# Kernel tuning notes

Hardware: AMD Instinct MI355X
Metric: run time of the kernel (lower is better)

The kernel has to match this reference:

```python
import jax, jax.numpy as jnp
import numpy as np

N = 100000   # nodes
E = 1600000  # edges (before self-loops)
H1, C1 = 8, 16   # conv1: heads=8, out_channels=16
H2, C2 = 1, 1    # conv2: heads=1, out_channels=1
NEG_SLOPE = 0.2
EPS = 1e-16


def setup_inputs() -> dict:
    key = jax.random.key(0)
    ks = jax.random.split(key, 10)
    s = 0.3
    return {
        "x": jax.random.normal(ks[0], (N, 1), jnp.float32),
        "edge_index": jax.random.randint(ks[1], (2, E), 0, N, dtype=jnp.int64),
        "W1": jax.random.normal(ks[2], (1, H1 * C1), jnp.float32) * s,
        "att_src1": jax.random.normal(ks[3], (1, H1, C1), jnp.float32) * s,
        "att_dst1": jax.random.normal(ks[4], (1, H1, C1), jnp.float32) * s,
        "b1": jax.random.normal(ks[5], (H1 * C1,), jnp.float32) * s,
        "W2": jax.random.normal(ks[6], (H1 * C1, H2 * C2), jnp.float32) * s,
        "att_src2": jax.random.normal(ks[7], (1, H2, C2), jnp.float32) * s,
        "att_dst2": jax.random.normal(ks[8], (1, H2, C2), jnp.float32) * s,
        "b2": jax.random.normal(ks[9], (C2,), jnp.float32) * s,
    }


def gat_conv(x, src, dst, W, att_src, att_dst, bias, heads, ch, concat):
    # Linear projection, split into heads: [N, H, C]
    h = (x @ W).reshape(-1, heads, ch)
    # Per-node attention logits: [N, H]
    a_src = (h * att_src).sum(-1)
    a_dst = (h * att_dst).sum(-1)
    # Edge-wise score with LeakyReLU: [E, H]
    e = jax.nn.leaky_relu(a_src[src] + a_dst[dst], NEG_SLOPE)
    # Segment softmax over incoming edges of each dst node
    m = jax.ops.segment_max(e, dst, num_segments=N)
    ex = jnp.exp(e - m[dst])
    denom = jax.ops.segment_sum(ex, dst, num_segments=N)
    alpha = ex / (denom[dst] + EPS)                      # [E, H]
    # Weighted scatter-add aggregation: [N, H, C]
    out = jax.ops.segment_sum(h[src] * alpha[:, :, None], dst, num_segments=N)
    out = out.reshape(-1, heads * ch) if concat else out.mean(axis=1)
    return out + bias


def reference(x, edge_index, W1, att_src1, att_dst1, b1, W2, att_src2, att_dst2, b2):
    # PyG GATConv default add_self_loops=True
    loop = jnp.arange(N, dtype=edge_index.dtype)
    src = jnp.concatenate([edge_index[0], loop])
    dst = jnp.concatenate([edge_index[1], loop])
    # dropout p=0.6 is identity in eval mode
    h = gat_conv(x, src, dst, W1, att_src1, att_dst1, b1, H1, C1, concat=True)
    h = jax.nn.elu(h)
    out = gat_conv(h, src, dst, W2, att_src2, att_dst2, b2, H2, C2, concat=False)
    return out  # [N, 1]
```

## Files before the change

### kernel.cpp

```cpp
#include <hip/hip_runtime.h>

#define NEG_SLOPE 0.2f
#define EPSV 1e-16f
#define NHEADS 8
#define NCH 16
#define BKT_SHIFT 8
#define BKT_NODES 256
#define CAP 8192
#define BIN_EPB 4096
#define MAX_BKT 512

__global__ __launch_bounds__(512) void gat_setup_kernel(
        const float* __restrict__ W1, const float* __restrict__ as1,
        const float* __restrict__ ad1, float* __restrict__ S1,
        float* __restrict__ D1, int* __restrict__ bkt_cnt, int nbuckets) {
    int t = threadIdx.x;
    for (int i = t; i < nbuckets; i += 512) bkt_cnt[i] = 0;
    if (t < NHEADS) {
        float s = 0.f, d = 0.f;
        for (int c = 0; c < NCH; ++c) {
            float w = W1[t * NCH + c];
            s += w * as1[t * NCH + c];
            d += w * ad1[t * NCH + c];
        }
        S1[t] = s;
        D1[t] = d;
    }
}

__global__ __launch_bounds__(256) void gat_bin_kernel(
        const int* __restrict__ ei, int E, int nbuckets,
        int* __restrict__ bkt_cnt, unsigned int* __restrict__ binned) {
    __shared__ int hist[MAX_BKT];
    __shared__ int gbase[MAX_BKT];
    int t = threadIdx.x;
    for (int i = t; i < nbuckets; i += 256) hist[i] = 0;
    __syncthreads();
    int base = blockIdx.x * BIN_EPB;
    int lr[BIN_EPB / 256];
#pragma unroll
    for (int k = 0; k < BIN_EPB / 1024; ++k) {
        int idx = base + k * 1024 + t * 4;
        if (idx + 3 < E) {
            int4 d4 = *(const int4*)(ei + E + idx);
            lr[4 * k + 0] = atomicAdd(&hist[d4.x >> BKT_SHIFT], 1);
            lr[4 * k + 1] = atomicAdd(&hist[d4.y >> BKT_SHIFT], 1);
            lr[4 * k + 2] = atomicAdd(&hist[d4.z >> BKT_SHIFT], 1);
            lr[4 * k + 3] = atomicAdd(&hist[d4.w >> BKT_SHIFT], 1);
        } else {
            for (int u = 0; u < 4; ++u)
                if (idx + u < E)
                    lr[4 * k + u] = atomicAdd(&hist[ei[E + idx + u] >> BKT_SHIFT], 1);
        }
    }
    __syncthreads();
    for (int i = t; i < nbuckets; i += 256) {
        int c = hist[i];
        gbase[i] = c ? (i * CAP + atomicAdd(&bkt_cnt[i], c)) : 0;
    }
    __syncthreads();
#pragma unroll
    for (int k = 0; k < BIN_EPB / 1024; ++k) {
        int idx = base + k * 1024 + t * 4;
        if (idx + 3 < E) {
            int4 s4 = *(const int4*)(ei + idx);
            int4 d4 = *(const int4*)(ei + E + idx);
            binned[gbase[d4.x >> BKT_SHIFT] + lr[4 * k + 0]] =
                ((unsigned int)s4.x << BKT_SHIFT) | (unsigned int)(d4.x & (BKT_NODES - 1));
            binned[gbase[d4.y >> BKT_SHIFT] + lr[4 * k + 1]] =
                ((unsigned int)s4.y << BKT_SHIFT) | (unsigned int)(d4.y & (BKT_NODES - 1));
            binned[gbase[d4.z >> BKT_SHIFT] + lr[4 * k + 2]] =
                ((unsigned int)s4.z << BKT_SHIFT) | (unsigned int)(d4.z & (BKT_NODES - 1));
            binned[gbase[d4.w >> BKT_SHIFT] + lr[4 * k + 3]] =
                ((unsigned int)s4.w << BKT_SHIFT) | (unsigned int)(d4.w & (BKT_NODES - 1));
        } else {
            for (int u = 0; u < 4; ++u)
                if (idx + u < E) {
                    unsigned int s = (unsigned int)ei[idx + u];
                    int d = ei[E + idx + u];
                    binned[gbase[d >> BKT_SHIFT] + lr[4 * k + u]] =
                        (s << BKT_SHIFT) | (unsigned int)(d & (BKT_NODES - 1));
                }
        }
    }
}

__global__ __launch_bounds__(256) void gat_gather1_kernel(
        int N, const float* __restrict__ x,
        unsigned int* __restrict__ binned, const int* __restrict__ bkt_cnt,
        const float* __restrict__ S1g, const float* __restrict__ D1g,
        const float* __restrict__ W1, const float* __restrict__ b1,
        const float* __restrict__ W2, float* __restrict__ h2out,
        int* __restrict__ row_start, int* __restrict__ row_deg) {
    __shared__ unsigned int ed[CAP];
    __shared__ int cnt[BKT_NODES];
    __shared__ int off[BKT_NODES];
    __shared__ int cur[BKT_NODES];
    __shared__ float xloc[BKT_NODES];
    int b = blockIdx.x, t = threadIdx.x;
    int node = (b << BKT_SHIFT) + t;
    xloc[t] = (node < N) ? x[node] : 0.f;
    cnt[t] = 0;
    __syncthreads();
    int nE = bkt_cnt[b]; if (nE > CAP) nE = CAP;
    const unsigned int* bb = binned + (size_t)b * CAP;
    for (int j0 = 0; j0 < nE; j0 += 1024) {
        int idx = j0 + t * 4;
        if (idx + 3 < nE) {
            uint4 q = *(const uint4*)(bb + idx);
            atomicAdd(&cnt[q.x & (BKT_NODES - 1)], 1);
            atomicAdd(&cnt[q.y & (BKT_NODES - 1)], 1);
            atomicAdd(&cnt[q.z & (BKT_NODES - 1)], 1);
            atomicAdd(&cnt[q.w & (BKT_NODES - 1)], 1);
        } else {
            for (int u = 0; u < 4; ++u)
                if (idx + u < nE) atomicAdd(&cnt[bb[idx + u] & (BKT_NODES - 1)], 1);
        }
    }
    __syncthreads();
    int c = cnt[t];
    off[t] = c;
    __syncthreads();
    for (int o = 1; o < 256; o <<= 1) {
        int v = (t >= o) ? off[t - o] : 0;
        __syncthreads();
        off[t] += v;
        __syncthreads();
    }
    int o_excl = off[t] - c;
    off[t] = o_excl;
    cur[t] = o_excl;
    __syncthreads();
    for (int j0 = 0; j0 < nE; j0 += 1024) {
        int idx = j0 + t * 4;
        if (idx + 3 < nE) {
            uint4 q = *(const uint4*)(bb + idx);
            ed[atomicAdd(&cur[q.x & (BKT_NODES - 1)], 1)] = q.x >> BKT_SHIFT;
            ed[atomicAdd(&cur[q.y & (BKT_NODES - 1)], 1)] = q.y >> BKT_SHIFT;
            ed[atomicAdd(&cur[q.z & (BKT_NODES - 1)], 1)] = q.z >> BKT_SHIFT;
            ed[atomicAdd(&cur[q.w & (BKT_NODES - 1)], 1)] = q.w >> BKT_SHIFT;
        } else {
            for (int u = 0; u < 4; ++u)
                if (idx + u < nE) {
                    unsigned int v = bb[idx + u];
                    ed[atomicAdd(&cur[v & (BKT_NODES - 1)], 1)] = v >> BKT_SHIFT;
                }
        }
    }
    __syncthreads();
    for (int j0 = 0; j0 < nE; j0 += 1024) {
        int idx = j0 + t * 4;
        if (idx + 3 < nE) {
            *(uint4*)(binned + (size_t)b * CAP + idx) = *(const uint4*)(ed + idx);
        } else {
            for (int u = 0; u < 4; ++u)
                if (idx + u < nE) binned[(size_t)b * CAP + idx + u] = ed[idx + u];
        }
    }
    if (node < N) {
        row_start[node] = b * CAP + o_excl;
        row_deg[node] = c;
    }
    float S1[NHEADS], A[NHEADS], den[NHEADS], num[NHEADS];
    float xn = xloc[t];
#pragma unroll
    for (int h = 0; h < NHEADS; ++h) {
        S1[h] = S1g[h];
        A[h] = xn * D1g[h];
        float e = xn * S1[h] + A[h];
        e = e > 0.f ? e : NEG_SLOPE * e;
        float ex = __expf(e);
        den[h] = ex + EPSV;
        num[h] = ex * xn;
    }
    int j = 0;
    for (; j + 4 <= c; j += 4) {
        unsigned int e0 = ed[o_excl + j + 0], e1 = ed[o_excl + j + 1];
        unsigned int e2 = ed[o_excl + j + 2], e3 = ed[o_excl + j + 3];
        float x0 = x[e0], x1 = x[e1], x2 = x[e2], x3 = x[e3];
#pragma unroll
        for (int h = 0; h < NHEADS; ++h) {
            float ea = x0 * S1[h] + A[h]; ea = ea > 0.f ? ea : NEG_SLOPE * ea;
            float eb = x1 * S1[h] + A[h]; eb = eb > 0.f ? eb : NEG_SLOPE * eb;
            float ec = x2 * S1[h] + A[h]; ec = ec > 0.f ? ec : NEG_SLOPE * ec;
            float ee = x3 * S1[h] + A[h]; ee = ee > 0.f ? ee : NEG_SLOPE * ee;
            float fa = __expf(ea), fb = __expf(eb), fc = __expf(ec), fd = __expf(ee);
            den[h] += (fa + fb) + (fc + fd);
            num[h] += (fa * x0 + fb * x1) + (fc * x2 + fd * x3);
        }
    }
    for (; j < c; ++j) {
        unsigned int e0 = ed[o_excl + j];
        float x0 = x[e0];
#pragma unroll
        for (int h = 0; h < NHEADS; ++h) {
            float ea = x0 * S1[h] + A[h];
            ea = ea > 0.f ? ea : NEG_SLOPE * ea;
            float fa = __expf(ea);
            den[h] += fa;
            num[h] += fa * x0;
        }
    }
    if (node >= N) return;
    float acc = 0.f;
#pragma unroll
    for (int h = 0; h < NHEADS; ++h) {
        float z = num[h] / den[h];
#pragma unroll
        for (int cc = 0; cc < NCH; ++cc) {
            int k = h * NCH + cc;
            float vv = W1[k] * z + b1[k];
            vv = vv > 0.f ? vv : (__expf(vv) - 1.f);
            acc += vv * W2[k];
        }
    }
    h2out[node] = acc;
}

__global__ __launch_bounds__(256) void gat_gather2_kernel(
        int N, const float* __restrict__ h2,
        const unsigned int* __restrict__ binned,
        const int* __restrict__ row_start, const int* __restrict__ row_deg,
        const float* __restrict__ as2p, const float* __restrict__ ad2p,
        const float* __restrict__ b2, float* __restrict__ out) {
    int n = blockIdx.x * blockDim.x + threadIdx.x;
    if (n >= N) return;
    float a_s = as2p[0], a_d = ad2p[0];
    float hn = h2[n];
    float ad = hn * a_d;
    float e = hn * a_s + ad;
    e = e > 0.f ? e : NEG_SLOPE * e;
    float ex = __expf(e);
    float den = ex + EPSV;
    float num = ex * hn;
    int st = row_start[n], dg = row_deg[n];
    int j = 0;
    for (; j + 4 <= dg; j += 4) {
        unsigned int e0 = binned[st + j + 0], e1 = binned[st + j + 1];
        unsigned int e2 = binned[st + j + 2], e3 = binned[st + j + 3];
        float h0 = h2[e0], h1 = h2[e1], h3 = h2[e2], h4 = h2[e3];
        float ea = h0 * a_s + ad; ea = ea > 0.f ? ea : NEG_SLOPE * ea;
        float eb = h1 * a_s + ad; eb = eb > 0.f ? eb : NEG_SLOPE * eb;
        float ec = h3 * a_s + ad; ec = ec > 0.f ? ec : NEG_SLOPE * ec;
        float ee = h4 * a_s + ad; ee = ee > 0.f ? ee : NEG_SLOPE * ee;
        float fa = __expf(ea), fb = __expf(eb), fc = __expf(ec), fd = __expf(ee);
        den += (fa + fb) + (fc + fd);
        num += (fa * h0 + fb * h1) + (fc * h3 + fd * h4);
    }
    for (; j < dg; ++j) {
        unsigned int e0 = binned[st + j];
        float h0 = h2[e0];
        float ea = h0 * a_s + ad;
        ea = ea > 0.f ? ea : NEG_SLOPE * ea;
        float fa = __expf(ea);
        den += fa;
        num += fa * h0;
    }
    out[n] = num / den + b2[0];
}

extern "C" void kernel_launch(void* const* d_in, const int* in_sizes, int n_in,
                              void* d_out, int out_size, void* d_ws, size_t ws_size,
                              hipStream_t stream) {
    const float* x   = (const float*)d_in[0];
    const int*   ei  = (const int*)d_in[1];
    const float* W1  = (const float*)d_in[2];
    const float* as1 = (const float*)d_in[3];
    const float* ad1 = (const float*)d_in[4];
    const float* b1  = (const float*)d_in[5];
    const float* W2  = (const float*)d_in[6];
    const float* as2 = (const float*)d_in[7];
    const float* ad2 = (const float*)d_in[8];
    const float* b2  = (const float*)d_in[9];
    float* out = (float*)d_out;

    int N = in_sizes[0];
    int E = in_sizes[1] / 2;

    int nbuckets = (N + BKT_NODES - 1) >> BKT_SHIFT;
    int nbin     = (E + BIN_EPB - 1) / BIN_EPB;
    int nb       = (N + 255) / 256;

    float* S1        = (float*)d_ws;
    float* D1        = S1 + 8;
    float* h2        = D1 + 8;
    int*   row_start = (int*)(h2 + N);
    int*   row_deg   = row_start + N;
    int*   bkt_cnt   = row_deg + N;
    unsigned int* binned = (unsigned int*)(bkt_cnt + nbuckets);

    gat_setup_kernel<<<1, 512, 0, stream>>>(W1, as1, ad1, S1, D1,
                                            bkt_cnt, nbuckets);
    gat_bin_kernel<<<nbin, 256, 0, stream>>>(ei, E, nbuckets, bkt_cnt, binned);
    gat_gather1_kernel<<<nbuckets, 256, 0, stream>>>(N, x, binned, bkt_cnt,
                                                     S1, D1, W1, b1, W2, h2,
                                                     row_start, row_deg);
    gat_gather2_kernel<<<nb, 256, 0, stream>>>(N, h2, binned, row_start, row_deg,
                                               as2, ad2, b2, out);
}
```

Measured before the change: 132.5 us.

## Replace per-bucket CSR sort with edge-parallel shared-memory atomic aggregation

The per-bucket counting sort that built a CSR layout (count, scan, scatter to shared memory, write back to global) is removed from the first gather kernel. Both gather kernels now process a bucket's edges in edge-parallel fashion with 512 threads and accumulate softmax numerators and denominators into shared-memory arrays with float atomics. Gather2 also switches from per-node CSR traversal to the same per-bucket scheme, and the S1/D1 precompute moves into gather1. This drops the sort passes and row_start/row_deg buffers, but adds 16 shared-memory float atomics per edge in layer 1 and makes the summation order nondeterministic.

```diff
diff --git a/kernel.cpp b/kernel.cpp
--- a/kernel.cpp
+++ b/kernel.cpp
@@ -11,21 +11,9 @@
 #define MAX_BKT 512
 
 __global__ __launch_bounds__(512) void gat_setup_kernel(
-        const float* __restrict__ W1, const float* __restrict__ as1,
-        const float* __restrict__ ad1, float* __restrict__ S1,
-        float* __restrict__ D1, int* __restrict__ bkt_cnt, int nbuckets) {
+        int* __restrict__ bkt_cnt, int nbuckets) {
     int t = threadIdx.x;
     for (int i = t; i < nbuckets; i += 512) bkt_cnt[i] = 0;
-    if (t < NHEADS) {
-        float s = 0.f, d = 0.f;
-        for (int c = 0; c < NCH; ++c) {
-            float w = W1[t * NCH + c];
-            s += w * as1[t * NCH + c];
-            d += w * ad1[t * NCH + c];
-        }
-        S1[t] = s;
-        D1[t] = d;
-    }
 }
 
 __global__ __launch_bounds__(256) void gat_bin_kernel(
@@ -37,20 +25,20 @@
     for (int i = t; i < nbuckets; i += 256) hist[i] = 0;
     __syncthreads();
     int base = blockIdx.x * BIN_EPB;
-    int lr[BIN_EPB / 256];
-#pragma unroll
-    for (int k = 0; k < BIN_EPB / 1024; ++k) {
+    int lr[16];
+#pragma unroll
+    for (int k = 0; k < 4; ++k) {
         int idx = base + k * 1024 + t * 4;
         if (idx + 3 < E) {
             int4 d4 = *(const int4*)(ei + E + idx);
-            lr[4 * k + 0] = atomicAdd(&hist[d4.x >> BKT_SHIFT], 1);
-            lr[4 * k + 1] = atomicAdd(&hist[d4.y >> BKT_SHIFT], 1);
-            lr[4 * k + 2] = atomicAdd(&hist[d4.z >> BKT_SHIFT], 1);
-            lr[4 * k + 3] = atomicAdd(&hist[d4.w >> BKT_SHIFT], 1);
+            lr[4*k+0] = atomicAdd(&hist[d4.x >> BKT_SHIFT], 1);
+            lr[4*k+1] = atomicAdd(&hist[d4.y >> BKT_SHIFT], 1);
+            lr[4*k+2] = atomicAdd(&hist[d4.z >> BKT_SHIFT], 1);
+            lr[4*k+3] = atomicAdd(&hist[d4.w >> BKT_SHIFT], 1);
         } else {
             for (int u = 0; u < 4; ++u)
                 if (idx + u < E)
-                    lr[4 * k + u] = atomicAdd(&hist[ei[E + idx + u] >> BKT_SHIFT], 1);
+                    lr[4*k+u] = atomicAdd(&hist[ei[E + idx + u] >> BKT_SHIFT], 1);
         }
     }
     __syncthreads();
@@ -60,203 +48,163 @@
     }
     __syncthreads();
 #pragma unroll
-    for (int k = 0; k < BIN_EPB / 1024; ++k) {
+    for (int k = 0; k < 4; ++k) {
         int idx = base + k * 1024 + t * 4;
         if (idx + 3 < E) {
             int4 s4 = *(const int4*)(ei + idx);
             int4 d4 = *(const int4*)(ei + E + idx);
-            binned[gbase[d4.x >> BKT_SHIFT] + lr[4 * k + 0]] =
-                ((unsigned int)s4.x << BKT_SHIFT) | (unsigned int)(d4.x & (BKT_NODES - 1));
-            binned[gbase[d4.y >> BKT_SHIFT] + lr[4 * k + 1]] =
-                ((unsigned int)s4.y << BKT_SHIFT) | (unsigned int)(d4.y & (BKT_NODES - 1));
-            binned[gbase[d4.z >> BKT_SHIFT] + lr[4 * k + 2]] =
-                ((unsigned int)s4.z << BKT_SHIFT) | (unsigned int)(d4.z & (BKT_NODES - 1));
-            binned[gbase[d4.w >> BKT_SHIFT] + lr[4 * k + 3]] =
-                ((unsigned int)s4.w << BKT_SHIFT) | (unsigned int)(d4.w & (BKT_NODES - 1));
+            binned[gbase[d4.x >> BKT_SHIFT] + lr[4*k+0]] =
+                ((unsigned)s4.x << BKT_SHIFT) | (unsigned)(d4.x & (BKT_NODES-1));
+            binned[gbase[d4.y >> BKT_SHIFT] + lr[4*k+1]] =
+                ((unsigned)s4.y << BKT_SHIFT) | (unsigned)(d4.y & (BKT_NODES-1));
+            binned[gbase[d4.z >> BKT_SHIFT] + lr[4*k+2]] =
+                ((unsigned)s4.z << BKT_SHIFT) | (unsigned)(d4.z & (BKT_NODES-1));
+            binned[gbase[d4.w >> BKT_SHIFT] + lr[4*k+3]] =
+                ((unsigned)s4.w << BKT_SHIFT) | (unsigned)(d4.w & (BKT_NODES-1));
         } else {
             for (int u = 0; u < 4; ++u)
                 if (idx + u < E) {
-                    unsigned int s = (unsigned int)ei[idx + u];
+                    unsigned s = (unsigned)ei[idx + u];
                     int d = ei[E + idx + u];
-                    binned[gbase[d >> BKT_SHIFT] + lr[4 * k + u]] =
-                        (s << BKT_SHIFT) | (unsigned int)(d & (BKT_NODES - 1));
+                    binned[gbase[d >> BKT_SHIFT] + lr[4*k+u]] =
+                        (s << BKT_SHIFT) | (unsigned)(d & (BKT_NODES-1));
                 }
         }
     }
 }
 
-__global__ __launch_bounds__(256) void gat_gather1_kernel(
+__global__ __launch_bounds__(512) void gat_gather1_kernel(
         int N, const float* __restrict__ x,
-        unsigned int* __restrict__ binned, const int* __restrict__ bkt_cnt,
-        const float* __restrict__ S1g, const float* __restrict__ D1g,
-        const float* __restrict__ W1, const float* __restrict__ b1,
-        const float* __restrict__ W2, float* __restrict__ h2out,
-        int* __restrict__ row_start, int* __restrict__ row_deg) {
-    __shared__ unsigned int ed[CAP];
-    __shared__ int cnt[BKT_NODES];
-    __shared__ int off[BKT_NODES];
-    __shared__ int cur[BKT_NODES];
+        const unsigned int* __restrict__ binned, const int* __restrict__ bkt_cnt,
+        const float* __restrict__ W1, const float* __restrict__ as1,
+        const float* __restrict__ ad1, const float* __restrict__ b1,
+        const float* __restrict__ W2, float* __restrict__ h2out) {
+    __shared__ float den[BKT_NODES][NHEADS];
+    __shared__ float num[BKT_NODES][NHEADS];
     __shared__ float xloc[BKT_NODES];
+    __shared__ float S1s[NHEADS], D1s[NHEADS];
     int b = blockIdx.x, t = threadIdx.x;
-    int node = (b << BKT_SHIFT) + t;
-    xloc[t] = (node < N) ? x[node] : 0.f;
-    cnt[t] = 0;
-    __syncthreads();
+    if (t < NHEADS) {
+        float s = 0.f, d = 0.f;
+        for (int c = 0; c < NCH; ++c) {
+            float w = W1[t * NCH + c];
+            s += w * as1[t * NCH + c];
+            d += w * ad1[t * NCH + c];
+        }
+        S1s[t] = s; D1s[t] = d;
+    }
+    __syncthreads();
+    int node = (b << BKT_SHIFT) + (t & (BKT_NODES - 1));
+    if (t < BKT_NODES) {
+        float xn = (node < N) ? x[node] : 0.f;
+        xloc[t] = xn;
+#pragma unroll
+        for (int h = 0; h < NHEADS; ++h) {
+            float e = xn * S1s[h] + xn * D1s[h];
+            e = e > 0.f ? e : NEG_SLOPE * e;
+            float ex = __expf(e);
+            den[t][h] = ex + EPSV;
+            num[t][h] = ex * xn;
+        }
+    }
+    __syncthreads();
+    float S1[NHEADS], D1[NHEADS];
+#pragma unroll
+    for (int h = 0; h < NHEADS; ++h) { S1[h] = S1s[h]; D1[h] = D1s[h]; }
     int nE = bkt_cnt[b]; if (nE > CAP) nE = CAP;
     const unsigned int* bb = binned + (size_t)b * CAP;
-    for (int j0 = 0; j0 < nE; j0 += 1024) {
+    for (int j0 = 0; j0 < nE; j0 += 2048) {
         int idx = j0 + t * 4;
+        unsigned v[4];
+        int nv;
         if (idx + 3 < nE) {
             uint4 q = *(const uint4*)(bb + idx);
-            atomicAdd(&cnt[q.x & (BKT_NODES - 1)], 1);
-            atomicAdd(&cnt[q.y & (BKT_NODES - 1)], 1);
-            atomicAdd(&cnt[q.z & (BKT_NODES - 1)], 1);
-            atomicAdd(&cnt[q.w & (BKT_NODES - 1)], 1);
-        } else {
-            for (int u = 0; u < 4; ++u)
-                if (idx + u < nE) atomicAdd(&cnt[bb[idx + u] & (BKT_NODES - 1)], 1);
-        }
-    }
-    __syncthreads();
-    int c = cnt[t];
-    off[t] = c;
-    __syncthreads();
-    for (int o = 1; o < 256; o <<= 1) {
-        int v = (t >= o) ? off[t - o] : 0;
-        __syncthreads();
-        off[t] += v;
-        __syncthreads();
-    }
-    int o_excl = off[t] - c;
-    off[t] = o_excl;
-    cur[t] = o_excl;
-    __syncthreads();
-    for (int j0 = 0; j0 < nE; j0 += 1024) {
+            v[0] = q.x; v[1] = q.y; v[2] = q.z; v[3] = q.w; nv = 4;
+        } else {
+            nv = nE - idx; if (nv < 0) nv = 0; if (nv > 4) nv = 4;
+            for (int u = 0; u < nv; ++u) v[u] = bb[idx + u];
+        }
+        for (int u = 0; u < nv; ++u) {
+            unsigned s = v[u] >> BKT_SHIFT;
+            int dl = v[u] & (BKT_NODES - 1);
+            float xs = x[s];
+            float xd = xloc[dl];
+#pragma unroll
+            for (int h = 0; h < NHEADS; ++h) {
+                float e = xs * S1[h] + xd * D1[h];
+                e = e > 0.f ? e : NEG_SLOPE * e;
+                float f = __expf(e);
+                atomicAdd(&den[dl][h], f);
+                atomicAdd(&num[dl][h], f * xs);
+            }
+        }
+    }
+    __syncthreads();
+    if (t < BKT_NODES && node < N) {
+        float acc = 0.f;
+#pragma unroll
+        for (int h = 0; h < NHEADS; ++h) {
+            float z = num[t][h] / den[t][h];
+#pragma unroll
+            for (int cc = 0; cc < NCH; ++cc) {
+                int k = h * NCH + cc;
+                float vv = W1[k] * z + b1[k];
+                vv = vv > 0.f ? vv : (__expf(vv) - 1.f);
+                acc += vv * W2[k];
+            }
+        }
+        h2out[node] = acc;
+    }
+}
+
+__global__ __launch_bounds__(512) void gat_gather2_kernel(
+        int N, const float* __restrict__ h2,
+        const unsigned int* __restrict__ binned, const int* __restrict__ bkt_cnt,
+        const float* __restrict__ as2p, const float* __restrict__ ad2p,
+        const float* __restrict__ b2, float* __restrict__ out) {
+    __shared__ float den2[BKT_NODES];
+    __shared__ float num2[BKT_NODES];
+    __shared__ float hloc[BKT_NODES];
+    int b = blockIdx.x, t = threadIdx.x;
+    float a_s = as2p[0], a_d = ad2p[0];
+    int node = (b << BKT_SHIFT) + (t & (BKT_NODES - 1));
+    if (t < BKT_NODES) {
+        float hn = (node < N) ? h2[node] : 0.f;
+        hloc[t] = hn;
+        float e = hn * a_s + hn * a_d;
+        e = e > 0.f ? e : NEG_SLOPE * e;
+        float ex = __expf(e);
+        den2[t] = ex + EPSV;
+        num2[t] = ex * hn;
+    }
+    __syncthreads();
+    int nE = bkt_cnt[b]; if (nE > CAP) nE = CAP;
+    const unsigned int* bb = binned + (size_t)b * CAP;
+    for (int j0 = 0; j0 < nE; j0 += 2048) {
         int idx = j0 + t * 4;
+        unsigned v[4];
+        int nv;
         if (idx + 3 < nE) {
             uint4 q = *(const uint4*)(bb + idx);
-            ed[atomicAdd(&cur[q.x & (BKT_NODES - 1)], 1)] = q.x >> BKT_SHIFT;
-            ed[atomicAdd(&cur[q.y & (BKT_NODES - 1)], 1)] = q.y >> BKT_SHIFT;
-            ed[atomicAdd(&cur[q.z & (BKT_NODES - 1)], 1)] = q.z >> BKT_SHIFT;
-            ed[atomicAdd(&cur[q.w & (BKT_NODES - 1)], 1)] = q.w >> BKT_SHIFT;
-        } else {
-            for (int u = 0; u < 4; ++u)
-                if (idx + u < nE) {
-                    unsigned int v = bb[idx + u];
-                    ed[atomicAdd(&cur[v & (BKT_NODES - 1)], 1)] = v >> BKT_SHIFT;
-                }
-        }
-    }
-    __syncthreads();
-    for (int j0 = 0; j0 < nE; j0 += 1024) {
-        int idx = j0 + t * 4;
-        if (idx + 3 < nE) {
-            *(uint4*)(binned + (size_t)b * CAP + idx) = *(const uint4*)(ed + idx);
-        } else {
-            for (int u = 0; u < 4; ++u)
-                if (idx + u < nE) binned[(size_t)b * CAP + idx + u] = ed[idx + u];
-        }
-    }
-    if (node < N) {
-        row_start[node] = b * CAP + o_excl;
-        row_deg[node] = c;
-    }
-    float S1[NHEADS], A[NHEADS], den[NHEADS], num[NHEADS];
-    float xn = xloc[t];
-#pragma unroll
-    for (int h = 0; h < NHEADS; ++h) {
-        S1[h] = S1g[h];
-        A[h] = xn * D1g[h];
-        float e = xn * S1[h] + A[h];
-        e = e > 0.f ? e : NEG_SLOPE * e;
-        float ex = __expf(e);
-        den[h] = ex + EPSV;
-        num[h] = ex * xn;
-    }
-    int j = 0;
-    for (; j + 4 <= c; j += 4) {
-        unsigned int e0 = ed[o_excl + j + 0], e1 = ed[o_excl + j + 1];
-        unsigned int e2 = ed[o_excl + j + 2], e3 = ed[o_excl + j + 3];
-        float x0 = x[e0], x1 = x[e1], x2 = x[e2], x3 = x[e3];
-#pragma unroll
-        for (int h = 0; h < NHEADS; ++h) {
-            float ea = x0 * S1[h] + A[h]; ea = ea > 0.f ? ea : NEG_SLOPE * ea;
-            float eb = x1 * S1[h] + A[h]; eb = eb > 0.f ? eb : NEG_SLOPE * eb;
-            float ec = x2 * S1[h] + A[h]; ec = ec > 0.f ? ec : NEG_SLOPE * ec;
-            float ee = x3 * S1[h] + A[h]; ee = ee > 0.f ? ee : NEG_SLOPE * ee;
-            float fa = __expf(ea), fb = __expf(eb), fc = __expf(ec), fd = __expf(ee);
-            den[h] += (fa + fb) + (fc + fd);
-            num[h] += (fa * x0 + fb * x1) + (fc * x2 + fd * x3);
-        }
-    }
-    for (; j < c; ++j) {
-        unsigned int e0 = ed[o_excl + j];
-        float x0 = x[e0];
-#pragma unroll
-        for (int h = 0; h < NHEADS; ++h) {
-            float ea = x0 * S1[h] + A[h];
-            ea = ea > 0.f ? ea : NEG_SLOPE * ea;
-            float fa = __expf(ea);
-            den[h] += fa;
-            num[h] += fa * x0;
-        }
-    }
-    if (node >= N) return;
-    float acc = 0.f;
-#pragma unroll
-    for (int h = 0; h < NHEADS; ++h) {
-        float z = num[h] / den[h];
-#pragma unroll
-        for (int cc = 0; cc < NCH; ++cc) {
-            int k = h * NCH + cc;
-            float vv = W1[k] * z + b1[k];
-            vv = vv > 0.f ? vv : (__expf(vv) - 1.f);
-            acc += vv * W2[k];
-        }
-    }
-    h2out[node] = acc;
-}
-
-__global__ __launch_bounds__(256) void gat_gather2_kernel(
-        int N, const float* __restrict__ h2,
-        const unsigned int* __restrict__ binned,
-        const int* __restrict__ row_start, const int* __restrict__ row_deg,
-        const float* __restrict__ as2p, const float* __restrict__ ad2p,
-        const float* __restrict__ b2, float* __restrict__ out) {
-    int n = blockIdx.x * blockDim.x + threadIdx.x;
-    if (n >= N) return;
-    float a_s = as2p[0], a_d = ad2p[0];
-    float hn = h2[n];
-    float ad = hn * a_d;
-    float e = hn * a_s + ad;
-    e = e > 0.f ? e : NEG_SLOPE * e;
-    float ex = __expf(e);
-    float den = ex + EPSV;
-    float num = ex * hn;
-    int st = row_start[n], dg = row_deg[n];
-    int j = 0;
-    for (; j + 4 <= dg; j += 4) {
-        unsigned int e0 = binned[st + j + 0], e1 = binned[st + j + 1];
-        unsigned int e2 = binned[st + j + 2], e3 = binned[st + j + 3];
-        float h0 = h2[e0], h1 = h2[e1], h3 = h2[e2], h4 = h2[e3];
-        float ea = h0 * a_s + ad; ea = ea > 0.f ? ea : NEG_SLOPE * ea;
-        float eb = h1 * a_s + ad; eb = eb > 0.f ? eb : NEG_SLOPE * eb;
-        float ec = h3 * a_s + ad; ec = ec > 0.f ? ec : NEG_SLOPE * ec;
-        float ee = h4 * a_s + ad; ee = ee > 0.f ? ee : NEG_SLOPE * ee;
-        float fa = __expf(ea), fb = __expf(eb), fc = __expf(ec), fd = __expf(ee);
-        den += (fa + fb) + (fc + fd);
-        num += (fa * h0 + fb * h1) + (fc * h3 + fd * h4);
-    }
-    for (; j < dg; ++j) {
-        unsigned int e0 = binned[st + j];
-        float h0 = h2[e0];
-        float ea = h0 * a_s + ad;
-        ea = ea > 0.f ? ea : NEG_SLOPE * ea;
-        float fa = __expf(ea);
-        den += fa;
-        num += fa * h0;
-    }
-    out[n] = num / den + b2[0];
+            v[0] = q.x; v[1] = q.y; v[2] = q.z; v[3] = q.w; nv = 4;
+        } else {
+            nv = nE - idx; if (nv < 0) nv = 0; if (nv > 4) nv = 4;
+            for (int u = 0; u < nv; ++u) v[u] = bb[idx + u];
+        }
+        for (int u = 0; u < nv; ++u) {
+            unsigned s = v[u] >> BKT_SHIFT;
+            int dl = v[u] & (BKT_NODES - 1);
+            float hs = h2[s];
+            float e = hs * a_s + hloc[dl] * a_d;
+            e = e > 0.f ? e : NEG_SLOPE * e;
+            float f = __expf(e);
+            atomicAdd(&den2[dl], f);
+            atomicAdd(&num2[dl], f * hs);
+        }
+    }
+    __syncthreads();
+    if (t < BKT_NODES && node < N)
+        out[node] = num2[t] / den2[t] + b2[0];
 }
 
 extern "C" void kernel_launch(void* const* d_in, const int* in_sizes, int n_in,
@@ -279,22 +227,15 @@
 
     int nbuckets = (N + BKT_NODES - 1) >> BKT_SHIFT;
     int nbin     = (E + BIN_EPB - 1) / BIN_EPB;
-    int nb       = (N + 255) / 256;
-
-    float* S1        = (float*)d_ws;
-    float* D1        = S1 + 8;
-    float* h2        = D1 + 8;
-    int*   row_start = (int*)(h2 + N);
-    int*   row_deg   = row_start + N;
-    int*   bkt_cnt   = row_deg + N;
+
+    float* h2      = (float*)d_ws;
+    int*   bkt_cnt = (int*)(h2 + N);
     unsigned int* binned = (unsigned int*)(bkt_cnt + nbuckets);
 
-    gat_setup_kernel<<<1, 512, 0, stream>>>(W1, as1, ad1, S1, D1,
-                                            bkt_cnt, nbuckets);
+    gat_setup_kernel<<<1, 512, 0, stream>>>(bkt_cnt, nbuckets);
     gat_bin_kernel<<<nbin, 256, 0, stream>>>(ei, E, nbuckets, bkt_cnt, binned);
-    gat_gather1_kernel<<<nbuckets, 256, 0, stream>>>(N, x, binned, bkt_cnt,
-                                                     S1, D1, W1, b1, W2, h2,
-                                                     row_start, row_deg);
-    gat_gather2_kernel<<<nb, 256, 0, stream>>>(N, h2, binned, row_start, row_deg,
-                                               as2, ad2, b2, out);
-}
+    gat_gather1_kernel<<<nbuckets, 512, 0, stream>>>(N, x, binned, bkt_cnt,
+                                                     W1, as1, ad1, b1, W2, h2);
+    gat_gather2_kernel<<<nbuckets, 512, 0, stream>>>(N, h2, binned, bkt_cnt,
+                                                     as2, ad2, b2, out);
+}
```

Result: slower. 301.8 us (+127.7%).

## Replace bucketed binning with fixed-slot per-node adjacency and overflow list

Applied to the files above, without the earlier changes.

Drops the two-pass bucket binning and the in-shared-memory per-bucket sort. Edges are now scattered straight into fixed 48-slot rows per destination node using global atomics on a degree array, and any excess goes to a small overflow list. The gather kernels become plain per-node kernels that read the slot rows with vector loads, and the setup kernel is replaced by a memset plus in-block computation of the head coefficients. This trades contention-heavy global atomics and scattered writes for fewer passes. It risks slow linear scans of the overflow list for high-degree nodes, and it silently drops edges if the overflow list fills.

```diff
diff --git a/kernel.cpp b/kernel.cpp
--- a/kernel.cpp
+++ b/kernel.cpp
@@ -4,18 +4,56 @@
 #define EPSV 1e-16f
 #define NHEADS 8
 #define NCH 16
-#define BKT_SHIFT 8
-#define BKT_NODES 256
-#define CAP 8192
-#define BIN_EPB 4096
-#define MAX_BKT 512
-
-__global__ __launch_bounds__(512) void gat_setup_kernel(
+#define SLOT 48
+#define OVF_CAP 8192
+#define SCAT_EPB 4096
+
+__global__ __launch_bounds__(256) void gat_scatter_kernel(
+        const int* __restrict__ ei, int E,
+        int* __restrict__ deg, int* __restrict__ ovf_cnt,
+        unsigned long long* __restrict__ ovf,
+        unsigned int* __restrict__ binned) {
+    int t = threadIdx.x;
+    int base = blockIdx.x * SCAT_EPB;
+#pragma unroll
+    for (int k = 0; k < 4; ++k) {
+        int idx = base + k * 1024 + t * 4;
+        int sv[4], dv[4], ne;
+        if (idx + 3 < E) {
+            int4 s4 = *(const int4*)(ei + idx);
+            int4 d4 = *(const int4*)(ei + E + idx);
+            sv[0] = s4.x; sv[1] = s4.y; sv[2] = s4.z; sv[3] = s4.w;
+            dv[0] = d4.x; dv[1] = d4.y; dv[2] = d4.z; dv[3] = d4.w;
+            ne = 4;
+        } else {
+            ne = E - idx; if (ne < 0) ne = 0; if (ne > 4) ne = 4;
+            for (int u = 0; u < ne; ++u) { sv[u] = ei[idx + u]; dv[u] = ei[E + idx + u]; }
+        }
+#pragma unroll
+        for (int u = 0; u < 4; ++u) {
+            if (u >= ne) break;
+            int d = dv[u];
+            int r = atomicAdd(&deg[d], 1);
+            if (r < SLOT) {
+                binned[(size_t)d * SLOT + r] = (unsigned)sv[u];
+            } else {
+                int o = atomicAdd(ovf_cnt, 1);
+                if (o < OVF_CAP)
+                    ovf[o] = ((unsigned long long)(unsigned)sv[u] << 32) | (unsigned)d;
+            }
+        }
+    }
+}
+
+__global__ __launch_bounds__(256) void gat_gather1_kernel(
+        int N, const float* __restrict__ x,
+        const unsigned int* __restrict__ binned, const int* __restrict__ deg,
+        const int* __restrict__ ovf_cnt, const unsigned long long* __restrict__ ovf,
         const float* __restrict__ W1, const float* __restrict__ as1,
-        const float* __restrict__ ad1, float* __restrict__ S1,
-        float* __restrict__ D1, int* __restrict__ bkt_cnt, int nbuckets) {
+        const float* __restrict__ ad1, const float* __restrict__ b1,
+        const float* __restrict__ W2, float* __restrict__ h2out) {
+    __shared__ float S1s[NHEADS], D1s[NHEADS];
     int t = threadIdx.x;
-    for (int i = t; i < nbuckets; i += 512) bkt_cnt[i] = 0;
     if (t < NHEADS) {
         float s = 0.f, d = 0.f;
         for (int c = 0; c < NCH; ++c) {
@@ -23,161 +61,32 @@
             s += w * as1[t * NCH + c];
             d += w * ad1[t * NCH + c];
         }
-        S1[t] = s;
-        D1[t] = d;
-    }
-}
-
-__global__ __launch_bounds__(256) void gat_bin_kernel(
-        const int* __restrict__ ei, int E, int nbuckets,
-        int* __restrict__ bkt_cnt, unsigned int* __restrict__ binned) {
-    __shared__ int hist[MAX_BKT];
-    __shared__ int gbase[MAX_BKT];
-    int t = threadIdx.x;
-    for (int i = t; i < nbuckets; i += 256) hist[i] = 0;
+        S1s[t] = s; D1s[t] = d;
+    }
     __syncthreads();
-    int base = blockIdx.x * BIN_EPB;
-    int lr[BIN_EPB / 256];
-#pragma unroll
-    for (int k = 0; k < BIN_EPB / 1024; ++k) {
-        int idx = base + k * 1024 + t * 4;
-        if (idx + 3 < E) {
-            int4 d4 = *(const int4*)(ei + E + idx);
-            lr[4 * k + 0] = atomicAdd(&hist[d4.x >> BKT_SHIFT], 1);
-            lr[4 * k + 1] = atomicAdd(&hist[d4.y >> BKT_SHIFT], 1);
-            lr[4 * k + 2] = atomicAdd(&hist[d4.z >> BKT_SHIFT], 1);
-            lr[4 * k + 3] = atomicAdd(&hist[d4.w >> BKT_SHIFT], 1);
-        } else {
-            for (int u = 0; u < 4; ++u)
-                if (idx + u < E)
-                    lr[4 * k + u] = atomicAdd(&hist[ei[E + idx + u] >> BKT_SHIFT], 1);
-        }
-    }
-    __syncthreads();
-    for (int i = t; i < nbuckets; i += 256) {
-        int c = hist[i];
-        gbase[i] = c ? (i * CAP + atomicAdd(&bkt_cnt[i], c)) : 0;
-    }
-    __syncthreads();
-#pragma unroll
-    for (int k = 0; k < BIN_EPB / 1024; ++k) {
-        int idx = base + k * 1024 + t * 4;
-        if (idx + 3 < E) {
-            int4 s4 = *(const int4*)(ei + idx);
-            int4 d4 = *(const int4*)(ei + E + idx);
-            binned[gbase[d4.x >> BKT_SHIFT] + lr[4 * k + 0]] =
-                ((unsigned int)s4.x << BKT_SHIFT) | (unsigned int)(d4.x & (BKT_NODES - 1));
-            binned[gbase[d4.y >> BKT_SHIFT] + lr[4 * k + 1]] =
-                ((unsigned int)s4.y << BKT_SHIFT) | (unsigned int)(d4.y & (BKT_NODES - 1));
-            binned[gbase[d4.z >> BKT_SHIFT] + lr[4 * k + 2]] =
-                ((unsigned int)s4.z << BKT_SHIFT) | (unsigned int)(d4.z & (BKT_NODES - 1));
-            binned[gbase[d4.w >> BKT_SHIFT] + lr[4 * k + 3]] =
-                ((unsigned int)s4.w << BKT_SHIFT) | (unsigned int)(d4.w & (BKT_NODES - 1));
-        } else {
-            for (int u = 0; u < 4; ++u)
-                if (idx + u < E) {
-                    unsigned int s = (unsigned int)ei[idx + u];
-                    int d = ei[E + idx + u];
-                    binned[gbase[d >> BKT_SHIFT] + lr[4 * k + u]] =
-                        (s << BKT_SHIFT) | (unsigned int)(d & (BKT_NODES - 1));
-                }
-        }
-    }
-}
-
-__global__ __launch_bounds__(256) void gat_gather1_kernel(
-        int N, const float* __restrict__ x,
-        unsigned int* __restrict__ binned, const int* __restrict__ bkt_cnt,
-        const float* __restrict__ S1g, const float* __restrict__ D1g,
-        const float* __restrict__ W1, const float* __restrict__ b1,
-        const float* __restrict__ W2, float* __restrict__ h2out,
-        int* __restrict__ row_start, int* __restrict__ row_deg) {
-    __shared__ unsigned int ed[CAP];
-    __shared__ int cnt[BKT_NODES];
-    __shared__ int off[BKT_NODES];
-    __shared__ int cur[BKT_NODES];
-    __shared__ float xloc[BKT_NODES];
-    int b = blockIdx.x, t = threadIdx.x;
-    int node = (b << BKT_SHIFT) + t;
-    xloc[t] = (node < N) ? x[node] : 0.f;
-    cnt[t] = 0;
-    __syncthreads();
-    int nE = bkt_cnt[b]; if (nE > CAP) nE = CAP;
-    const unsigned int* bb = binned + (size_t)b * CAP;
-    for (int j0 = 0; j0 < nE; j0 += 1024) {
-        int idx = j0 + t * 4;
-        if (idx + 3 < nE) {
-            uint4 q = *(const uint4*)(bb + idx);
-            atomicAdd(&cnt[q.x & (BKT_NODES - 1)], 1);
-            atomicAdd(&cnt[q.y & (BKT_NODES - 1)], 1);
-            atomicAdd(&cnt[q.z & (BKT_NODES - 1)], 1);
-            atomicAdd(&cnt[q.w & (BKT_NODES - 1)], 1);
-        } else {
-            for (int u = 0; u < 4; ++u)
-                if (idx + u < nE) atomicAdd(&cnt[bb[idx + u] & (BKT_NODES - 1)], 1);
-        }
-    }
-    __syncthreads();
-    int c = cnt[t];
-    off[t] = c;
-    __syncthreads();
-    for (int o = 1; o < 256; o <<= 1) {
-        int v = (t >= o) ? off[t - o] : 0;
-        __syncthreads();
-        off[t] += v;
-        __syncthreads();
-    }
-    int o_excl = off[t] - c;
-    off[t] = o_excl;
-    cur[t] = o_excl;
-    __syncthreads();
-    for (int j0 = 0; j0 < nE; j0 += 1024) {
-        int idx = j0 + t * 4;
-        if (idx + 3 < nE) {
-            uint4 q = *(const uint4*)(bb + idx);
-            ed[atomicAdd(&cur[q.x & (BKT_NODES - 1)], 1)] = q.x >> BKT_SHIFT;
-            ed[atomicAdd(&cur[q.y & (BKT_NODES - 1)], 1)] = q.y >> BKT_SHIFT;
-            ed[atomicAdd(&cur[q.z & (BKT_NODES - 1)], 1)] = q.z >> BKT_SHIFT;
-            ed[atomicAdd(&cur[q.w & (BKT_NODES - 1)], 1)] = q.w >> BKT_SHIFT;
-        } else {
-            for (int u = 0; u < 4; ++u)
-                if (idx + u < nE) {
-                    unsigned int v = bb[idx + u];
-                    ed[atomicAdd(&cur[v & (BKT_NODES - 1)], 1)] = v >> BKT_SHIFT;
-                }
-        }
-    }
-    __syncthreads();
-    for (int j0 = 0; j0 < nE; j0 += 1024) {
-        int idx = j0 + t * 4;
-        if (idx + 3 < nE) {
-            *(uint4*)(binned + (size_t)b * CAP + idx) = *(const uint4*)(ed + idx);
-        } else {
-            for (int u = 0; u < 4; ++u)
-                if (idx + u < nE) binned[(size_t)b * CAP + idx + u] = ed[idx + u];
-        }
-    }
-    if (node < N) {
-        row_start[node] = b * CAP + o_excl;
-        row_deg[node] = c;
-    }
-    float S1[NHEADS], A[NHEADS], den[NHEADS], num[NHEADS];
-    float xn = xloc[t];
+    int n = blockIdx.x * 256 + t;
+    if (n >= N) return;
+    float S1[NHEADS], D1[NHEADS], den[NHEADS], num[NHEADS];
+    float xn = x[n];
 #pragma unroll
     for (int h = 0; h < NHEADS; ++h) {
-        S1[h] = S1g[h];
-        A[h] = xn * D1g[h];
-        float e = xn * S1[h] + A[h];
+        S1[h] = S1s[h]; D1[h] = D1s[h];
+        float e = xn * S1[h] + xn * D1[h];
         e = e > 0.f ? e : NEG_SLOPE * e;
         float ex = __expf(e);
         den[h] = ex + EPSV;
         num[h] = ex * xn;
     }
+    int dg = deg[n];
+    int c = dg < SLOT ? dg : SLOT;
+    const unsigned int* bb = binned + (size_t)n * SLOT;
+    float A[NHEADS];
+#pragma unroll
+    for (int h = 0; h < NHEADS; ++h) A[h] = xn * D1[h];
     int j = 0;
     for (; j + 4 <= c; j += 4) {
-        unsigned int e0 = ed[o_excl + j + 0], e1 = ed[o_excl + j + 1];
-        unsigned int e2 = ed[o_excl + j + 2], e3 = ed[o_excl + j + 3];
-        float x0 = x[e0], x1 = x[e1], x2 = x[e2], x3 = x[e3];
+        uint4 q = *(const uint4*)(bb + j);
+        float x0 = x[q.x], x1 = x[q.y], x2 = x[q.z], x3 = x[q.w];
 #pragma unroll
         for (int h = 0; h < NHEADS; ++h) {
             float ea = x0 * S1[h] + A[h]; ea = ea > 0.f ? ea : NEG_SLOPE * ea;
@@ -190,8 +99,8 @@
         }
     }
     for (; j < c; ++j) {
-        unsigned int e0 = ed[o_excl + j];
-        float x0 = x[e0];
+        unsigned s = bb[j];
+        float x0 = x[s];
 #pragma unroll
         for (int h = 0; h < NHEADS; ++h) {
             float ea = x0 * S1[h] + A[h];
@@ -201,7 +110,23 @@
             num[h] += fa * x0;
         }
     }
-    if (node >= N) return;
+    if (dg > SLOT) {
+        int on = *ovf_cnt; if (on > OVF_CAP) on = OVF_CAP;
+        for (int i = 0; i < on; ++i) {
+            unsigned long long e64 = ovf[i];
+            if ((int)(e64 & 0xFFFFFFFFu) == n) {
+                float x0 = x[(unsigned)(e64 >> 32)];
+#pragma unroll
+                for (int h = 0; h < NHEADS; ++h) {
+                    float ea = x0 * S1[h] + A[h];
+                    ea = ea > 0.f ? ea : NEG_SLOPE * ea;
+                    float fa = __expf(ea);
+                    den[h] += fa;
+                    num[h] += fa * x0;
+                }
+            }
+        }
+    }
     float acc = 0.f;
 #pragma unroll
     for (int h = 0; h < NHEADS; ++h) {
@@ -214,16 +139,16 @@
             acc += vv * W2[k];
         }
     }
-    h2out[node] = acc;
+    h2out[n] = acc;
 }
 
 __global__ __launch_bounds__(256) void gat_gather2_kernel(
         int N, const float* __restrict__ h2,
-        const unsigned int* __restrict__ binned,
-        const int* __restrict__ row_start, const int* __restrict__ row_deg,
+        const unsigned int* __restrict__ binned, const int* __restrict__ deg,
+        const int* __restrict__ ovf_cnt, const unsigned long long* __restrict__ ovf,
         const float* __restrict__ as2p, const float* __restrict__ ad2p,
         const float* __restrict__ b2, float* __restrict__ out) {
-    int n = blockIdx.x * blockDim.x + threadIdx.x;
+    int n = blockIdx.x * 256 + threadIdx.x;
     if (n >= N) return;
     float a_s = as2p[0], a_d = ad2p[0];
     float hn = h2[n];
@@ -233,12 +158,13 @@
     float ex = __expf(e);
     float den = ex + EPSV;
     float num = ex * hn;
-    int st = row_start[n], dg = row_deg[n];
+    int dg = deg[n];
+    int c = dg < SLOT ? dg : SLOT;
+    const unsigned int* bb = binned + (size_t)n * SLOT;
     int j = 0;
-    for (; j + 4 <= dg; j += 4) {
-        unsigned int e0 = binned[st + j + 0], e1 = binned[st + j + 1];
-        unsigned int e2 = binned[st + j + 2], e3 = binned[st + j + 3];
-        float h0 = h2[e0], h1 = h2[e1], h3 = h2[e2], h4 = h2[e3];
+    for (; j + 4 <= c; j += 4) {
+        uint4 q = *(const uint4*)(bb + j);
+        float h0 = h2[q.x], h1 = h2[q.y], h3 = h2[q.z], h4 = h2[q.w];
         float ea = h0 * a_s + ad; ea = ea > 0.f ? ea : NEG_SLOPE * ea;
         float eb = h1 * a_s + ad; eb = eb > 0.f ? eb : NEG_SLOPE * eb;
         float ec = h3 * a_s + ad; ec = ec > 0.f ? ec : NEG_SLOPE * ec;
@@ -247,14 +173,27 @@
         den += (fa + fb) + (fc + fd);
         num += (fa * h0 + fb * h1) + (fc * h3 + fd * h4);
     }
-    for (; j < dg; ++j) {
-        unsigned int e0 = binned[st + j];
-        float h0 = h2[e0];
+    for (; j < c; ++j) {
+        float h0 = h2[bb[j]];
         float ea = h0 * a_s + ad;
         ea = ea > 0.f ? ea : NEG_SLOPE * ea;
         float fa = __expf(ea);
         den += fa;
         num += fa * h0;
+    }
+    if (dg > SLOT) {
+        int on = *ovf_cnt; if (on > OVF_CAP) on = OVF_CAP;
+        for (int i = 0; i < on; ++i) {
+            unsigned long long e64 = ovf[i];
+            if ((int)(e64 & 0xFFFFFFFFu) == n) {
+                float h0 = h2[(unsigned)(e64 >> 32)];
+                float ea = h0 * a_s + ad;
+                ea = ea > 0.f ? ea : NEG_SLOPE * ea;
+                float fa = __expf(ea);
+                den += fa;
+                num += fa * h0;
+            }
+        }
     }
     out[n] = num / den + b2[0];
 }
@@ -277,24 +216,19 @@
     int N = in_sizes[0];
     int E = in_sizes[1] / 2;
 
-    int nbuckets = (N + BKT_NODES - 1) >> BKT_SHIFT;
-    int nbin     = (E + BIN_EPB - 1) / BIN_EPB;
-    int nb       = (N + 255) / 256;
-
-    float* S1        = (float*)d_ws;
-    float* D1        = S1 + 8;
-    float* h2        = D1 + 8;
-    int*   row_start = (int*)(h2 + N);
-    int*   row_deg   = row_start + N;
-    int*   bkt_cnt   = row_deg + N;
-    unsigned int* binned = (unsigned int*)(bkt_cnt + nbuckets);
-
-    gat_setup_kernel<<<1, 512, 0, stream>>>(W1, as1, ad1, S1, D1,
-                                            bkt_cnt, nbuckets);
-    gat_bin_kernel<<<nbin, 256, 0, stream>>>(ei, E, nbuckets, bkt_cnt, binned);
-    gat_gather1_kernel<<<nbuckets, 256, 0, stream>>>(N, x, binned, bkt_cnt,
-                                                     S1, D1, W1, b1, W2, h2,
-                                                     row_start, row_deg);
-    gat_gather2_kernel<<<nb, 256, 0, stream>>>(N, h2, binned, row_start, row_deg,
-                                               as2, ad2, b2, out);
-}
+    unsigned long long* ovf = (unsigned long long*)d_ws;
+    float* h2      = (float*)(ovf + OVF_CAP);
+    int*   deg     = (int*)(h2 + N);
+    int*   ovf_cnt = deg + N;
+    unsigned int* binned = (unsigned int*)(ovf_cnt + 1);
+
+    int nscat = (E + SCAT_EPB - 1) / SCAT_EPB;
+    int ngath = (N + 255) / 256;
+
+    hipMemsetAsync(deg, 0, (size_t)(N + 1) * sizeof(int), stream);
+    gat_scatter_kernel<<<nscat, 256, 0, stream>>>(ei, E, deg, ovf_cnt, ovf, binned);
+    gat_gather1_kernel<<<ngath, 256, 0, stream>>>(N, x, binned, deg, ovf_cnt, ovf,
+                                                  W1, as1, ad1, b1, W2, h2);
+    gat_gather2_kernel<<<ngath, 256, 0, stream>>>(N, h2, binned, deg, ovf_cnt, ovf,
+                                                  as2, ad2, b2, out);
+}
```

Measured after the change: 209.9 us. +58.4%, slower.
